# Kernel tuning notes

Measured on AMD Instinct MI355X. Metric: run time of the kernel, lower is better.

The kernel has to match this reference:

```python
import jax, jax.numpy as jnp
import numpy as np

K = 3
ACCEPTANCE_RADIUS = 0.1
CONFIDENCE_THRESHOLD = 0.05
CORRESPONDENCE_THRESHOLD = 3
NUM_REFINEMENT_STEPS = 5
EPS = 1e-5


def _pair_dist2(ref_pts, src_pts):
    # ref: (..., M, 3), src: (..., N, 3) -> squared distances (..., M, N)
    r2 = jnp.sum(ref_pts * ref_pts, axis=-1)[..., :, None]
    s2 = jnp.sum(src_pts * src_pts, axis=-1)[..., None, :]
    cross = jnp.einsum('...mc,...nc->...mn', ref_pts, src_pts)
    return r2 + s2 - 2.0 * cross


def _svd_rigid(H, cr, cs):
    # H = sum w (src-cs)(ref-cr)^T, torch convention H = U S V^T; R = V E U^T
    U, S, Vh = jnp.linalg.svd(H)
    V = jnp.swapaxes(Vh, -1, -2)
    Ut = jnp.swapaxes(U, -1, -2)
    d = jnp.sign(jnp.linalg.det(V @ Ut))
    V = V.at[..., :, 2].multiply(d[..., None])  # E = diag(1,1,sign(det))
    R = V @ Ut
    t = cr - jnp.einsum('...cd,...d->...c', R, cs)
    return R, t


def _procrustes_batch(w, ref_pts, src_pts):
    # dense weighted Procrustes per patch; w: (B,M,N), ref: (B,M,3), src: (B,N,3)
    wn = w / (jnp.sum(w, axis=(1, 2), keepdims=True) + EPS)
    cr = jnp.einsum('bmn,bmc->bc', wn, ref_pts)
    cs = jnp.einsum('bmn,bnc->bc', wn, src_pts)
    refc = ref_pts - cr[:, None, :]
    srcc = src_pts - cs[:, None, :]
    A = jnp.einsum('bmn,bmd->bnd', wn, refc)
    H = jnp.einsum('bnc,bnd->bcd', srcc, A)  # (B,3,3)
    return _svd_rigid(H, cr, cs)


def _procrustes_global(w, ref_pts, src_pts):
    # single transform over all stacked correspondences (zero weights = absent)
    wn = w / (jnp.sum(w) + EPS)
    cr = jnp.einsum('bmn,bmc->c', wn, ref_pts)
    cs = jnp.einsum('bmn,bnc->c', wn, src_pts)
    refc = ref_pts - cr
    srcc = src_pts - cs
    A = jnp.einsum('bmn,bmd->bnd', wn, refc)
    H = jnp.einsum('bnc,bnd->cd', srcc, A)  # (3,3)
    return _svd_rigid(H, cr, cs)


def setup_inputs() -> dict:
    key = jax.random.key(0)
    kr, ks, kn = jax.random.split(key, 3)
    B, M, N = 128, 64, 64
    ref = jax.random.uniform(kr, (B, M, 3), jnp.float32)
    src = ref + 0.01 * jax.random.normal(ks, (B, N, 3), jnp.float32)
    # scores correlated with proximity so top-k/mutual selection yields real inliers
    d = jnp.sqrt(jnp.maximum(_pair_dist2(ref, src), 0.0))
    score_mat = 2.0 - 10.0 * d + 0.1 * jax.random.normal(kn, (B, M, N), jnp.float32)
    return {"ref_knn_points": ref, "src_knn_points": src, "score_mat": score_mat}


def reference(ref_knn_points, src_knn_points, score_mat):
    B, M, N = score_mat.shape
    exp_scores = jnp.exp(score_mat)

    # --- top-k selection along each dim + confidence threshold (mutual=True) ---
    _, ref_idx = jax.lax.top_k(exp_scores, K)                      # (B,M,K) over src dim
    bi = jnp.arange(B)[:, None, None]
    mi = jnp.arange(M)[None, :, None]
    ref_sel = jnp.zeros((B, M, N), bool).at[bi, mi, ref_idx].set(True)
    _, src_idx = jax.lax.top_k(jnp.swapaxes(exp_scores, 1, 2), K)  # (B,N,K) over ref dim
    ni = jnp.arange(N)[None, :, None]
    src_sel = jnp.swapaxes(jnp.zeros((B, N, M), bool).at[bi, ni, src_idx].set(True), 1, 2)
    conf = exp_scores > CONFIDENCE_THRESHOLD
    corr_mat = ref_sel & src_sel & conf
    w = exp_scores * corr_mat                                       # dense corr scores

    # --- per-patch candidate transforms (weighted Procrustes) ---
    Rb, tb = _procrustes_batch(w, ref_knn_points, src_knn_points)   # (B,3,3),(B,3)

    # --- verify every candidate transform against all correspondences ---
    moved = jnp.einsum('bnc,pdc->pbnd', src_knn_points, Rb) + tb[:, None, None, :]
    d2 = _pair_dist2(ref_knn_points[None], moved)                   # (P,B,M,N)
    r2 = ACCEPTANCE_RADIUS * ACCEPTANCE_RADIUS
    inlier = (d2 < r2) & corr_mat[None]
    counts = jnp.sum(inlier, axis=(1, 2, 3))
    valid = jnp.sum(corr_mat, axis=(1, 2)) >= CORRESPONDENCE_THRESHOLD
    counts = jnp.where(valid, counts, -1)
    best = jnp.argmax(counts)

    # --- iterative global refinement ---
    cur_w = w * inlier[best]
    R, t = _procrustes_global(cur_w, ref_knn_points, src_knn_points)
    for _ in range(NUM_REFINEMENT_STEPS - 1):
        moved = src_knn_points @ R.T + t                            # (B,N,3)
        d2 = _pair_dist2(ref_knn_points, moved)                     # (B,M,N)
        cur_w = w * (d2 < r2)
        R, t = _procrustes_global(cur_w, ref_knn_points, src_knn_points)

    transform = jnp.eye(4, dtype=R.dtype).at[:3, :3].set(R).at[:3, 3].set(t)
    return w, transform
```

## Files before the change

kernel.cpp:

```cpp
#include <hip/hip_runtime.h>
#include <math.h>

#define NB 128
#define NM 64
#define NN 64
#define KSEL 3
#define SLOTS (NM * KSEL)
#define TOTSLOTS (NB * SLOTS)
#define CONF_TH 0.05f
#define RAD2 0.01f
#define EPSV 1e-5
#define CBLK 48
#define CTHR 512

struct Slot {
  float4 s;
  float4 r;
};

struct Ws {
  Slot   pack[TOTSLOTS];
  float  Rb[NB * 9];
  float  tb[NB * 3];
  int    ncorr[NB];
  int    bestkey;
  int    bar_cnt;
  int    bar_gen;
  double partial[CBLK][16];
  float  cur[12];
};

__device__ __forceinline__ void mat3vec(const double H[3][3], const double v[3], double o[3]) {
  o[0] = H[0][0] * v[0] + H[0][1] * v[1] + H[0][2] * v[2];
  o[1] = H[1][0] * v[0] + H[1][1] * v[1] + H[1][2] * v[2];
  o[2] = H[2][0] * v[0] + H[2][1] * v[1] + H[2][2] * v[2];
}

__device__ __forceinline__ void cross3(const double a[3], const double b[3], double o[3]) {
  o[0] = a[1] * b[2] - a[2] * b[1];
  o[1] = a[2] * b[0] - a[0] * b[2];
  o[2] = a[0] * b[1] - a[1] * b[0];
}

__device__ void solve_rigid(const double* acc, float* Rf, float* tf) {
  double denom = acc[0] + EPSV;
  double cr[3], cs[3];
  for (int i = 0; i < 3; i++) { cr[i] = acc[1 + i] / denom; cs[i] = acc[4 + i] / denom; }
  double sig = acc[0] / denom;
  double H[3][3];
  for (int c = 0; c < 3; c++)
    for (int d = 0; d < 3; d++)
      H[c][d] = acc[7 + c * 3 + d] / denom - (2.0 - sig) * cs[c] * cr[d];

  double A[3][3], V[3][3] = {{1,0,0},{0,1,0},{0,0,1}};
  for (int i = 0; i < 3; i++)
    for (int j = 0; j < 3; j++) {
      double s = 0;
      for (int k = 0; k < 3; k++) s += H[k][i] * H[k][j];
      A[i][j] = s;
    }
  for (int sweep = 0; sweep < 15; sweep++) {
    for (int p = 0; p < 3; p++) {
      for (int q = p + 1; q < 3; q++) {
        double apq = A[p][q];
        if (fabs(apq) <= 1e-14 * (fabs(A[p][p]) + fabs(A[q][q]))) continue;
        double tau = (A[q][q] - A[p][p]) / (2.0 * apq);
        double tt = (tau >= 0.0) ? 1.0 / (tau + sqrt(1.0 + tau * tau))
                                 : 1.0 / (tau - sqrt(1.0 + tau * tau));
        double c = 1.0 / sqrt(1.0 + tt * tt), s = tt * c;
        for (int k = 0; k < 3; k++) {
          double akp = A[k][p], akq = A[k][q];
          A[k][p] = c * akp - s * akq;
          A[k][q] = s * akp + c * akq;
        }
        for (int k = 0; k < 3; k++) {
          double apk = A[p][k], aqk = A[q][k];
          A[p][k] = c * apk - s * aqk;
          A[q][k] = s * apk + c * aqk;
        }
        for (int k = 0; k < 3; k++) {
          double vkp = V[k][p], vkq = V[k][q];
          V[k][p] = c * vkp - s * vkq;
          V[k][q] = s * vkp + c * vkq;
        }
      }
    }
  }
  double lam[3] = {A[0][0], A[1][1], A[2][2]};
  int i0 = 0, i1 = 1, i2 = 2, tmp;
  if (lam[i0] < lam[i1]) { tmp = i0; i0 = i1; i1 = tmp; }
  if (lam[i0] < lam[i2]) { tmp = i0; i0 = i2; i2 = tmp; }
  if (lam[i1] < lam[i2]) { tmp = i1; i1 = i2; i2 = tmp; }

  double v1[3] = {V[0][i0], V[1][i0], V[2][i0]};
  double v2[3] = {V[0][i1], V[1][i1], V[2][i1]};
  double u1[3], u2[3];
  mat3vec(H, v1, u1);
  double n1 = sqrt(u1[0]*u1[0] + u1[1]*u1[1] + u1[2]*u1[2]);
  if (n1 > 1e-30) { u1[0] /= n1; u1[1] /= n1; u1[2] /= n1; }
  else { u1[0] = 1; u1[1] = 0; u1[2] = 0; }
  mat3vec(H, v2, u2);
  double d12 = u1[0]*u2[0] + u1[1]*u2[1] + u1[2]*u2[2];
  u2[0] -= d12 * u1[0]; u2[1] -= d12 * u1[1]; u2[2] -= d12 * u1[2];
  double n2 = sqrt(u2[0]*u2[0] + u2[1]*u2[1] + u2[2]*u2[2]);
  if (n2 > 1e-30) { u2[0] /= n2; u2[1] /= n2; u2[2] /= n2; }
  else {
    double ax[3] = { (fabs(u1[0]) < 0.9) ? 1.0 : 0.0, (fabs(u1[0]) < 0.9) ? 0.0 : 1.0, 0.0 };
    cross3(u1, ax, u2);
    double nn = sqrt(u2[0]*u2[0] + u2[1]*u2[1] + u2[2]*u2[2]);
    u2[0] /= nn; u2[1] /= nn; u2[2] /= nn;
  }
  double u3[3], v3[3];
  cross3(u1, u2, u3);
  cross3(v1, v2, v3);
  double Rd[3][3];
  for (int i = 0; i < 3; i++)
    for (int j = 0; j < 3; j++)
      Rd[i][j] = v1[i] * u1[j] + v2[i] * u2[j] + v3[i] * u3[j];
  for (int i = 0; i < 3; i++) {
    double t = cr[i] - (Rd[i][0] * cs[0] + Rd[i][1] * cs[1] + Rd[i][2] * cs[2]);
    tf[i] = (float)t;
    for (int j = 0; j < 3; j++) Rf[i * 3 + j] = (float)Rd[i][j];
  }
}

__device__ __forceinline__ void gbar(int* cnt, int* gen) {
  __syncthreads();
  if (threadIdx.x == 0) {
    int g = __hip_atomic_load(gen, __ATOMIC_RELAXED, __HIP_MEMORY_SCOPE_AGENT);
    __threadfence();
    int old = __hip_atomic_fetch_add(cnt, 1, __ATOMIC_ACQ_REL, __HIP_MEMORY_SCOPE_AGENT);
    if (old == CBLK - 1) {
      __hip_atomic_store(cnt, 0, __ATOMIC_RELAXED, __HIP_MEMORY_SCOPE_AGENT);
      __threadfence();
      __hip_atomic_fetch_add(gen, 1, __ATOMIC_ACQ_REL, __HIP_MEMORY_SCOPE_AGENT);
    } else {
      while (__hip_atomic_load(gen, __ATOMIC_ACQUIRE, __HIP_MEMORY_SCOPE_AGENT) == g)
        __builtin_amdgcn_s_sleep(1);
    }
  }
  __syncthreads();
}

__global__ __launch_bounds__(256) void kA(const float* __restrict__ ref,
                                          const float* __restrict__ src,
                                          const float* __restrict__ score,
                                          float* __restrict__ wout,
                                          Ws* __restrict__ ws) {
  const int b = blockIdx.x;
  const int tid = threadIdx.x;
  __shared__ float se[NM][NN + 1];
  __shared__ unsigned long long rowmask[NM], colmask[NN];
  __shared__ int rsel[NM][KSEL];
  __shared__ float red[16][SLOTS + 1];
  __shared__ double acc[16];
  __shared__ int scount;

  const float* sc = score + (size_t)b * NM * NN;
  for (int i = tid; i < NM * NN; i += 256)
    se[i >> 6][i & 63] = expf(sc[i]);
  if (tid == 0) scount = 0;
  __syncthreads();

  if (tid < NM) {
    const int m = tid;
    float v0 = -1e30f, v1 = -1e30f, v2 = -1e30f; int j0 = 0, j1 = 0, j2 = 0;
    for (int n = 0; n < NN; n++) {
      float v = se[m][n];
      if (v > v0) { v2 = v1; j2 = j1; v1 = v0; j1 = j0; v0 = v; j0 = n; }
      else if (v > v1) { v2 = v1; j2 = j1; v1 = v; j1 = n; }
      else if (v > v2) { v2 = v; j2 = n; }
    }
    rsel[m][0] = j0; rsel[m][1] = j1; rsel[m][2] = j2;
    rowmask[m] = (1ull << j0) | (1ull << j1) | (1ull << j2);
  } else if (tid < 128) {
    const int n = tid - 64;
    float v0 = -1e30f, v1 = -1e30f, v2 = -1e30f; int j0 = 0, j1 = 0, j2 = 0;
    for (int m = 0; m < NM; m++) {
      float v = se[m][n];
      if (v > v0) { v2 = v1; j2 = j1; v1 = v0; j1 = j0; v0 = v; j0 = m; }
      else if (v > v1) { v2 = v1; j2 = j1; v1 = v; j1 = m; }
      else if (v > v2) { v2 = v; j2 = m; }
    }
    colmask[n] = (1ull << j0) | (1ull << j1) | (1ull << j2);
  }
  __syncthreads();

  float* wo = wout + (size_t)b * NM * NN;
  for (int i = tid; i < NM * NN; i += 256) {
    int m = i >> 6, n = i & 63;
    float e = se[m][n];
    bool corr = ((rowmask[m] >> n) & 1ull) && ((colmask[n] >> m) & 1ull) && (e > CONF_TH);
    wo[i] = corr ? e : 0.0f;
  }

  if (tid < SLOTS) {
    int m = tid / 3;
    int k = tid - m * 3;
    int n = rsel[m][k];
    float e = se[m][n];
    bool corr = ((colmask[n] >> m) & 1ull) && (e > CONF_TH);
    float cw = corr ? e : 0.0f;
    float rx = ref[((size_t)b * NM + m) * 3 + 0];
    float ry = ref[((size_t)b * NM + m) * 3 + 1];
    float rz = ref[((size_t)b * NM + m) * 3 + 2];
    float sx = src[((size_t)b * NN + n) * 3 + 0];
    float sy = src[((size_t)b * NN + n) * 3 + 1];
    float sz = src[((size_t)b * NN + n) * 3 + 2];
    ws->pack[b * SLOTS + tid].s = make_float4(sx, sy, sz, cw);
    ws->pack[b * SLOTS + tid].r = make_float4(rx, ry, rz, 0.0f);
    if (corr) atomicAdd(&scount, 1);
    red[0][tid] = cw;
    red[1][tid] = cw * rx;  red[2][tid] = cw * ry;  red[3][tid] = cw * rz;
    red[4][tid] = cw * sx;  red[5][tid] = cw * sy;  red[6][tid] = cw * sz;
    red[7][tid]  = cw * sx * rx; red[8][tid]  = cw * sx * ry; red[9][tid]  = cw * sx * rz;
    red[10][tid] = cw * sy * rx; red[11][tid] = cw * sy * ry; red[12][tid] = cw * sy * rz;
    red[13][tid] = cw * sz * rx; red[14][tid] = cw * sz * ry; red[15][tid] = cw * sz * rz;
  }
  __syncthreads();
  if (tid < 16) {
    double s = 0;
    for (int i = 0; i < SLOTS; i++) s += (double)red[tid][i];
    acc[tid] = s;
  }
  __syncthreads();
  if (tid == 0) {
    float Rf[9], tf[3];
    solve_rigid(acc, Rf, tf);
    for (int i = 0; i < 9; i++) ws->Rb[b * 9 + i] = Rf[i];
    for (int i = 0; i < 3; i++) ws->tb[b * 3 + i] = tf[i];
    ws->ncorr[b] = scount;
    if (b == 0) { ws->bestkey = 0; ws->bar_cnt = 0; ws->bar_gen = 0; }
  }
}

__global__ __launch_bounds__(256) void kB(Ws* __restrict__ ws) {
  const int p = blockIdx.x;
  const int tid = threadIdx.x;
  float R[9], T[3];
#pragma unroll
  for (int i = 0; i < 9; i++) R[i] = ws->Rb[p * 9 + i];
#pragma unroll
  for (int i = 0; i < 3; i++) T[i] = ws->tb[p * 3 + i];

  int cnt = 0;
  for (int g = tid; g < TOTSLOTS; g += 256) {
    float4 S = ws->pack[g].s;
    float4 Rv = ws->pack[g].r;
    float sx = S.x, sy = S.y, sz = S.z;
    float rx = Rv.x, ry = Rv.y, rz = Rv.z;
    float mx = R[0] * sx + R[1] * sy + R[2] * sz + T[0];
    float my = R[3] * sx + R[4] * sy + R[5] * sz + T[1];
    float mz = R[6] * sx + R[7] * sy + R[8] * sz + T[2];
    float d2 = (rx * rx + ry * ry + rz * rz) + (mx * mx + my * my + mz * mz)
             - 2.0f * (rx * mx + ry * my + rz * mz);
    cnt += (S.w > 0.0f && d2 < RAD2) ? 1 : 0;
  }
  __shared__ int sred[256];
  sred[tid] = cnt;
  __syncthreads();
  for (int s = 128; s > 0; s >>= 1) {
    if (tid < s) sred[tid] += sred[tid + s];
    __syncthreads();
  }
  if (tid == 0) {
    int c = (ws->ncorr[p] >= 3) ? sred[0] : -1;
    int key = ((c + 1) << 8) | (127 - p);
    atomicMax(&ws->bestkey, key);
  }
}

__global__ __launch_bounds__(CTHR) void kC(float* __restrict__ outT,
                                           Ws* __restrict__ ws) {
  const int tid = threadIdx.x, bid = blockIdx.x;
  const int lane = tid & 63, wid = tid >> 6;
  __shared__ double lred[16][CTHR / 64];
  __shared__ double accs[16];
  __shared__ float sRt[12];

  const int g = bid * CTHR + tid;
  const float4 S  = ws->pack[g].s;
  const float4 Rv = ws->pack[g].r;
  const float sx = S.x, sy = S.y, sz = S.z, w0 = S.w;
  const float rx = Rv.x, ry = Rv.y, rz = Rv.z;
  const float rr = rx * rx + ry * ry + rz * rz;

  for (int iter = 0; iter < 5; iter++) {
    float Rm[12];
    if (iter == 0) {
      int p = 127 - (ws->bestkey & 0xFF);
#pragma unroll
      for (int i = 0; i < 9; i++) Rm[i] = ws->Rb[p * 9 + i];
#pragma unroll
      for (int i = 0; i < 3; i++) Rm[9 + i] = ws->tb[p * 3 + i];
    } else {
#pragma unroll
      for (int i = 0; i < 12; i++)
        Rm[i] = __hip_atomic_load(&ws->cur[i], __ATOMIC_RELAXED, __HIP_MEMORY_SCOPE_AGENT);
    }

    float mx = Rm[0] * sx + Rm[1] * sy + Rm[2] * sz + Rm[9];
    float my = Rm[3] * sx + Rm[4] * sy + Rm[5] * sz + Rm[10];
    float mz = Rm[6] * sx + Rm[7] * sy + Rm[8] * sz + Rm[11];
    float d2 = rr + (mx * mx + my * my + mz * mz)
             - 2.0f * (rx * mx + ry * my + rz * mz);
    float w_ = (d2 < RAD2) ? w0 : 0.0f;
    float wsx = w_ * sx, wsy = w_ * sy, wsz = w_ * sz;
    float la[16];
    la[0] = w_;
    la[1] = w_ * rx;  la[2] = w_ * ry;  la[3] = w_ * rz;
    la[4] = wsx;      la[5] = wsy;      la[6] = wsz;
    la[7]  = wsx * rx; la[8]  = wsx * ry; la[9]  = wsx * rz;
    la[10] = wsy * rx; la[11] = wsy * ry; la[12] = wsy * rz;
    la[13] = wsz * rx; la[14] = wsz * ry; la[15] = wsz * rz;

#pragma unroll
    for (int q = 0; q < 16; q++) {
      float v = la[q];
      for (int off = 32; off > 0; off >>= 1) v += __shfl_down(v, off);
      if (lane == 0) lred[q][wid] = (double)v;
    }
    __syncthreads();
    if (tid < 16) {
      double s = 0;
#pragma unroll
      for (int k = 0; k < CTHR / 64; k++) s += lred[tid][k];
      __hip_atomic_store(&ws->partial[bid][tid], s, __ATOMIC_RELAXED, __HIP_MEMORY_SCOPE_AGENT);
    }
    gbar(&ws->bar_cnt, &ws->bar_gen);

    if (bid == 0) {
      if (tid < 16) {
        double s = 0;
        for (int k = 0; k < CBLK; k++)
          s += __hip_atomic_load(&ws->partial[k][tid], __ATOMIC_RELAXED, __HIP_MEMORY_SCOPE_AGENT);
        accs[tid] = s;
      }
      __syncthreads();
      if (tid == 0) {
        float Rf[9], tf[3];
        solve_rigid(accs, Rf, tf);
#pragma unroll
        for (int i = 0; i < 9; i++) sRt[i] = Rf[i];
#pragma unroll
        for (int i = 0; i < 3; i++) sRt[9 + i] = tf[i];
        if (iter < 4) {
#pragma unroll
          for (int i = 0; i < 12; i++)
            __hip_atomic_store(&ws->cur[i], sRt[i], __ATOMIC_RELAXED, __HIP_MEMORY_SCOPE_AGENT);
        }
      }
      __syncthreads();
    }
    if (iter < 4) gbar(&ws->bar_cnt, &ws->bar_gen);
  }

  if (bid == 0 && tid == 0) {
    outT[0] = sRt[0]; outT[1] = sRt[1]; outT[2]  = sRt[2]; outT[3]  = sRt[9];
    outT[4] = sRt[3]; outT[5] = sRt[4]; outT[6]  = sRt[5]; outT[7]  = sRt[10];
    outT[8] = sRt[6]; outT[9] = sRt[7]; outT[10] = sRt[8]; outT[11] = sRt[11];
    outT[12] = 0.0f; outT[13] = 0.0f; outT[14] = 0.0f; outT[15] = 1.0f;
  }
}

extern "C" void kernel_launch(void* const* d_in, const int* in_sizes, int n_in,
                              void* d_out, int out_size, void* d_ws, size_t ws_size,
                              hipStream_t stream) {
  const float* ref   = (const float*)d_in[0];
  const float* src   = (const float*)d_in[1];
  const float* score = (const float*)d_in[2];
  float* w    = (float*)d_out;
  float* outT = (float*)d_out + (size_t)NB * NM * NN;
  Ws* ws = (Ws*)d_ws;

  kA<<<NB, 256, 0, stream>>>(ref, src, score, w, ws);
  kB<<<NB, 256, 0, stream>>>(ws);
  kC<<<CBLK, CTHR, 0, stream>>>(outT, ws);
}
```

Measured before the change: 199.9 us.

## Replace persistent grid barrier refinement kernel with per-iteration launches and last-block reduction

The single persistent refinement kernel, which synchronised its 48 blocks through a spin-wait global barrier twice per iteration, becomes five separate kernel launches. Each launch reduces its partial sums, and the last block to arrive, found with an atomic ticket counter, does the final reduction and the rigid solve. This removes the spin-barrier latency and the idle wait of the other blocks. In exchange it adds four more kernel launches and reloads the point data on each launch.

Measured after the change: 175.0 us. 1.14x faster.

```diff
diff --git a/kernel.cpp b/kernel.cpp
--- a/kernel.cpp
+++ b/kernel.cpp
@@ -12,6 +12,7 @@
 #define EPSV 1e-5
 #define CBLK 48
 #define CTHR 512
+#define ITERS 5
 
 struct Slot {
   float4 s;
@@ -24,8 +25,7 @@
   float  tb[NB * 3];
   int    ncorr[NB];
   int    bestkey;
-  int    bar_cnt;
-  int    bar_gen;
+  int    ticket[ITERS];
   double partial[CBLK][16];
   float  cur[12];
 };
@@ -124,24 +124,6 @@
   }
 }
 
-__device__ __forceinline__ void gbar(int* cnt, int* gen) {
-  __syncthreads();
-  if (threadIdx.x == 0) {
-    int g = __hip_atomic_load(gen, __ATOMIC_RELAXED, __HIP_MEMORY_SCOPE_AGENT);
-    __threadfence();
-    int old = __hip_atomic_fetch_add(cnt, 1, __ATOMIC_ACQ_REL, __HIP_MEMORY_SCOPE_AGENT);
-    if (old == CBLK - 1) {
-      __hip_atomic_store(cnt, 0, __ATOMIC_RELAXED, __HIP_MEMORY_SCOPE_AGENT);
-      __threadfence();
-      __hip_atomic_fetch_add(gen, 1, __ATOMIC_ACQ_REL, __HIP_MEMORY_SCOPE_AGENT);
-    } else {
-      while (__hip_atomic_load(gen, __ATOMIC_ACQUIRE, __HIP_MEMORY_SCOPE_AGENT) == g)
-        __builtin_amdgcn_s_sleep(1);
-    }
-  }
-  __syncthreads();
-}
-
 __global__ __launch_bounds__(256) void kA(const float* __restrict__ ref,
                                           const float* __restrict__ src,
                                           const float* __restrict__ score,
@@ -230,7 +212,10 @@
     for (int i = 0; i < 9; i++) ws->Rb[b * 9 + i] = Rf[i];
     for (int i = 0; i < 3; i++) ws->tb[b * 3 + i] = tf[i];
     ws->ncorr[b] = scount;
-    if (b == 0) { ws->bestkey = 0; ws->bar_cnt = 0; ws->bar_gen = 0; }
+    if (b == 0) {
+      ws->bestkey = 0;
+      for (int i = 0; i < ITERS; i++) ws->ticket[i] = 0;
+    }
   }
 }
 
@@ -270,96 +255,90 @@
   }
 }
 
-__global__ __launch_bounds__(CTHR) void kC(float* __restrict__ outT,
-                                           Ws* __restrict__ ws) {
+__global__ __launch_bounds__(CTHR) void kCiter(int iter, float* __restrict__ outT,
+                                               Ws* __restrict__ ws) {
   const int tid = threadIdx.x, bid = blockIdx.x;
   const int lane = tid & 63, wid = tid >> 6;
   __shared__ double lred[16][CTHR / 64];
   __shared__ double accs[16];
-  __shared__ float sRt[12];
+  __shared__ int amLast;
 
   const int g = bid * CTHR + tid;
   const float4 S  = ws->pack[g].s;
   const float4 Rv = ws->pack[g].r;
   const float sx = S.x, sy = S.y, sz = S.z, w0 = S.w;
   const float rx = Rv.x, ry = Rv.y, rz = Rv.z;
-  const float rr = rx * rx + ry * ry + rz * rz;
-
-  for (int iter = 0; iter < 5; iter++) {
-    float Rm[12];
-    if (iter == 0) {
-      int p = 127 - (ws->bestkey & 0xFF);
-#pragma unroll
-      for (int i = 0; i < 9; i++) Rm[i] = ws->Rb[p * 9 + i];
-#pragma unroll
-      for (int i = 0; i < 3; i++) Rm[9 + i] = ws->tb[p * 3 + i];
+
+  float Rm[12];
+  if (iter == 0) {
+    int p = 127 - (ws->bestkey & 0xFF);
+#pragma unroll
+    for (int i = 0; i < 9; i++) Rm[i] = ws->Rb[p * 9 + i];
+#pragma unroll
+    for (int i = 0; i < 3; i++) Rm[9 + i] = ws->tb[p * 3 + i];
+  } else {
+#pragma unroll
+    for (int i = 0; i < 12; i++) Rm[i] = ws->cur[i];
+  }
+
+  float mx = Rm[0] * sx + Rm[1] * sy + Rm[2] * sz + Rm[9];
+  float my = Rm[3] * sx + Rm[4] * sy + Rm[5] * sz + Rm[10];
+  float mz = Rm[6] * sx + Rm[7] * sy + Rm[8] * sz + Rm[11];
+  float d2 = (rx * rx + ry * ry + rz * rz) + (mx * mx + my * my + mz * mz)
+           - 2.0f * (rx * mx + ry * my + rz * mz);
+  float w_ = (d2 < RAD2) ? w0 : 0.0f;
+  float wsx = w_ * sx, wsy = w_ * sy, wsz = w_ * sz;
+  float la[16];
+  la[0] = w_;
+  la[1] = w_ * rx;  la[2] = w_ * ry;  la[3] = w_ * rz;
+  la[4] = wsx;      la[5] = wsy;      la[6] = wsz;
+  la[7]  = wsx * rx; la[8]  = wsx * ry; la[9]  = wsx * rz;
+  la[10] = wsy * rx; la[11] = wsy * ry; la[12] = wsy * rz;
+  la[13] = wsz * rx; la[14] = wsz * ry; la[15] = wsz * rz;
+
+#pragma unroll
+  for (int q = 0; q < 16; q++) {
+    float v = la[q];
+    for (int off = 32; off > 0; off >>= 1) v += __shfl_down(v, off);
+    if (lane == 0) lred[q][wid] = (double)v;
+  }
+  __syncthreads();
+  if (tid < 16) {
+    double s = 0;
+#pragma unroll
+    for (int k = 0; k < CTHR / 64; k++) s += lred[tid][k];
+    __hip_atomic_store(&ws->partial[bid][tid], s, __ATOMIC_RELEASE, __HIP_MEMORY_SCOPE_AGENT);
+  }
+  __syncthreads();
+  if (tid == 0) {
+    int old = __hip_atomic_fetch_add(&ws->ticket[iter], 1, __ATOMIC_ACQ_REL,
+                                     __HIP_MEMORY_SCOPE_AGENT);
+    amLast = (old == CBLK - 1);
+  }
+  __syncthreads();
+  if (!amLast) return;
+
+  if (tid < 16) {
+    double s = 0;
+    for (int k = 0; k < CBLK; k++)
+      s += __hip_atomic_load(&ws->partial[k][tid], __ATOMIC_RELAXED, __HIP_MEMORY_SCOPE_AGENT);
+    accs[tid] = s;
+  }
+  __syncthreads();
+  if (tid == 0) {
+    float Rf[9], tf[3];
+    solve_rigid(accs, Rf, tf);
+    if (iter < ITERS - 1) {
+#pragma unroll
+      for (int i = 0; i < 9; i++) ws->cur[i] = Rf[i];
+#pragma unroll
+      for (int i = 0; i < 3; i++) ws->cur[9 + i] = tf[i];
     } else {
-#pragma unroll
-      for (int i = 0; i < 12; i++)
-        Rm[i] = __hip_atomic_load(&ws->cur[i], __ATOMIC_RELAXED, __HIP_MEMORY_SCOPE_AGENT);
-    }
-
-    float mx = Rm[0] * sx + Rm[1] * sy + Rm[2] * sz + Rm[9];
-    float my = Rm[3] * sx + Rm[4] * sy + Rm[5] * sz + Rm[10];
-    float mz = Rm[6] * sx + Rm[7] * sy + Rm[8] * sz + Rm[11];
-    float d2 = rr + (mx * mx + my * my + mz * mz)
-             - 2.0f * (rx * mx + ry * my + rz * mz);
-    float w_ = (d2 < RAD2) ? w0 : 0.0f;
-    float wsx = w_ * sx, wsy = w_ * sy, wsz = w_ * sz;
-    float la[16];
-    la[0] = w_;
-    la[1] = w_ * rx;  la[2] = w_ * ry;  la[3] = w_ * rz;
-    la[4] = wsx;      la[5] = wsy;      la[6] = wsz;
-    la[7]  = wsx * rx; la[8]  = wsx * ry; la[9]  = wsx * rz;
-    la[10] = wsy * rx; la[11] = wsy * ry; la[12] = wsy * rz;
-    la[13] = wsz * rx; la[14] = wsz * ry; la[15] = wsz * rz;
-
-#pragma unroll
-    for (int q = 0; q < 16; q++) {
-      float v = la[q];
-      for (int off = 32; off > 0; off >>= 1) v += __shfl_down(v, off);
-      if (lane == 0) lred[q][wid] = (double)v;
-    }
-    __syncthreads();
-    if (tid < 16) {
-      double s = 0;
-#pragma unroll
-      for (int k = 0; k < CTHR / 64; k++) s += lred[tid][k];
-      __hip_atomic_store(&ws->partial[bid][tid], s, __ATOMIC_RELAXED, __HIP_MEMORY_SCOPE_AGENT);
-    }
-    gbar(&ws->bar_cnt, &ws->bar_gen);
-
-    if (bid == 0) {
-      if (tid < 16) {
-        double s = 0;
-        for (int k = 0; k < CBLK; k++)
-          s += __hip_atomic_load(&ws->partial[k][tid], __ATOMIC_RELAXED, __HIP_MEMORY_SCOPE_AGENT);
-        accs[tid] = s;
-      }
-      __syncthreads();
-      if (tid == 0) {
-        float Rf[9], tf[3];
-        solve_rigid(accs, Rf, tf);
-#pragma unroll
-        for (int i = 0; i < 9; i++) sRt[i] = Rf[i];
-#pragma unroll
-        for (int i = 0; i < 3; i++) sRt[9 + i] = tf[i];
-        if (iter < 4) {
-#pragma unroll
-          for (int i = 0; i < 12; i++)
-            __hip_atomic_store(&ws->cur[i], sRt[i], __ATOMIC_RELAXED, __HIP_MEMORY_SCOPE_AGENT);
-        }
-      }
-      __syncthreads();
-    }
-    if (iter < 4) gbar(&ws->bar_cnt, &ws->bar_gen);
-  }
-
-  if (bid == 0 && tid == 0) {
-    outT[0] = sRt[0]; outT[1] = sRt[1]; outT[2]  = sRt[2]; outT[3]  = sRt[9];
-    outT[4] = sRt[3]; outT[5] = sRt[4]; outT[6]  = sRt[5]; outT[7]  = sRt[10];
-    outT[8] = sRt[6]; outT[9] = sRt[7]; outT[10] = sRt[8]; outT[11] = sRt[11];
-    outT[12] = 0.0f; outT[13] = 0.0f; outT[14] = 0.0f; outT[15] = 1.0f;
+      outT[0] = Rf[0]; outT[1] = Rf[1]; outT[2]  = Rf[2]; outT[3]  = tf[0];
+      outT[4] = Rf[3]; outT[5] = Rf[4]; outT[6]  = Rf[5]; outT[7]  = tf[1];
+      outT[8] = Rf[6]; outT[9] = Rf[7]; outT[10] = Rf[8]; outT[11] = tf[2];
+      outT[12] = 0.0f; outT[13] = 0.0f; outT[14] = 0.0f; outT[15] = 1.0f;
+    }
   }
 }
 
@@ -375,5 +354,6 @@
 
   kA<<<NB, 256, 0, stream>>>(ref, src, score, w, ws);
   kB<<<NB, 256, 0, stream>>>(ws);
-  kC<<<CBLK, CTHR, 0, stream>>>(outT, ws);
-}
+  for (int it = 0; it < ITERS; ++it)
+    kCiter<<<CBLK, CTHR, 0, stream>>>(it, outT, ws);
+}
```
